# Performance work log

Hardware: AMD Instinct MI355X
Metric: run time of the kernel (lower is better)

## Reference

```python
import jax, jax.numpy as jnp
import numpy as np

B, T, D = 128, 256, 1024

def setup_inputs() -> dict:
    key = jax.random.key(0)
    ks = jax.random.split(key, 7)
    s = 1.0 / np.sqrt(D)
    return {
        "inputs": jax.random.normal(ks[0], (B, T, D), dtype=jnp.float32),
        "Wk": jax.random.uniform(ks[1], (D, D), jnp.float32, -s, s),
        "bk": jax.random.uniform(ks[2], (D,), jnp.float32, -s, s),
        "Wq": jax.random.uniform(ks[3], (D, D), jnp.float32, -s, s),
        "bq": jax.random.uniform(ks[4], (D,), jnp.float32, -s, s),
        "Wv": jax.random.uniform(ks[5], (D, D), jnp.float32, -s, s),
        "bv": jax.random.uniform(ks[6], (D,), jnp.float32, -s, s),
    }

def reference(inputs, Wk, bk, Wq, bq, Wv, bv):
    # torch.nn.Linear: y = x @ W.T + b
    keys = inputs @ Wk.T + bk        # [B, T, D]
    queries = inputs @ Wq.T + bq     # [B, T, D]
    values = inputs @ Wv.T + bv      # [B, T, D]
    scale = 1.0 / jnp.sqrt(jnp.float32(inputs.shape[-1]))
    scores = jnp.einsum('btd,bsd->bts', queries, keys) * scale  # [B, T, T]
    t = inputs.shape[1]
    causal = jnp.tril(jnp.ones((t, t), dtype=bool))
    scores = jnp.where(causal, scores, -jnp.inf)
    probs = jax.nn.softmax(scores, axis=-1)
    return jnp.einsum('bts,bsd->btd', probs, values)
```

## Files before the change

kernel.cpp:

```cpp
#include <hip/hip_runtime.h>
#include <hip/hip_bf16.h>


typedef __attribute__((ext_vector_type(4))) float f32x4;
typedef __attribute__((ext_vector_type(8))) short s16x8;
typedef unsigned short u16;

__device__ inline u16 f2bf(float f) {
    union { __hip_bfloat16 h; u16 u; } c;
    c.h = __float2bfloat16(f);
    return c.u;
}

__device__ __forceinline__ void stage16(const void* g, void* l) {
    __builtin_amdgcn_global_load_lds((const __attribute__((address_space(1))) void*)g,
                                     (__attribute__((address_space(3))) void*)l, 16, 0, 0);
}

#define MFMA(a_, b_, c_) (c_) = __builtin_amdgcn_mfma_f32_16x16x32_bf16((a_), (b_), (c_), 0, 0, 0)

__global__ __launch_bounds__(256) void cvt_f32_bf16(const float* __restrict__ in,
                                                    u16* __restrict__ out, int n4) {
    int stride = gridDim.x * blockDim.x;
    for (int i = blockIdx.x * blockDim.x + threadIdx.x; i < n4; i += stride) {
        float4 v = reinterpret_cast<const float4*>(in)[i];
        ushort4 o = make_ushort4(f2bf(v.x), f2bf(v.y), f2bf(v.z), f2bf(v.w));
        reinterpret_cast<ushort4*>(out)[i] = o;
    }
}

__global__ __launch_bounds__(512, 4) void qkv128(const u16* __restrict__ X, const u16* __restrict__ W3,
                                                 const float* __restrict__ biasK,
                                                 const float* __restrict__ biasQ,
                                                 const float* __restrict__ biasV,
                                                 u16* __restrict__ Kb, u16* __restrict__ Qb,
                                                 u16* __restrict__ Vt) {
    __shared__ char lds[49152];

    const int bid = blockIdx.x;
    const int swz = (bid & 7) * 384 + (bid >> 3);
    const int mt = swz / 12, nt2 = swz % 12;
    const int nmat = nt2 >> 2, ncol = nt2 & 3;
    const u16* Asrc = X + (size_t)mt * 128 * 1024;
    const u16* Bsrc = W3 + (size_t)nmat * 1048576 + (size_t)ncol * 256 * 1024;

    const int tid  = threadIdx.x;
    const int lane = tid & 63, w = tid >> 6;
    const int wr = w >> 2, wc = w & 3;
    const int l15 = lane & 15, l16 = lane >> 4;

    const int rdoff = l15 * 64 + (((l16 ^ ((l15 >> 1) & 3)) & 3) << 4);
    const int aoff = wr * 4096 + rdoff;
    const int boff = 8192 + wc * 4096 + rdoff;

    const int srow = tid >> 2, sslot = tid & 3;
    const int scol = (sslot ^ ((srow >> 1) & 3)) * 8;
    const u16* asrcp  = Asrc + (size_t)srow * 1024 + scol;
    const u16* bsrcp0 = Bsrc + (size_t)srow * 1024 + scol;
    const u16* bsrcp1 = Bsrc + (size_t)(srow + 128) * 1024 + scol;

    f32x4 acc[4][4] = {};

#define STG(u_) do {                                                              \
        char* bb_ = lds + (((u_) & 1) * 24576) + w * 1024;                        \
        const size_t ko_ = (size_t)(u_) * 32;                                     \
        stage16(asrcp  + ko_, bb_);                                               \
        stage16(bsrcp0 + ko_, bb_ + 8192);                                        \
        stage16(bsrcp1 + ko_, bb_ + 16384);                                       \
    } while (0)

    STG(0);
    asm volatile("s_waitcnt vmcnt(0)" ::: "memory");
    __builtin_amdgcn_s_barrier();

    for (int u = 0; u < 32; ++u) {
        if (u < 31) STG(u + 1);
        const char* bp = lds + (u & 1) * 24576;
        s16x8 a[4], b[4];
#pragma unroll
        for (int fm = 0; fm < 4; ++fm) a[fm] = *(const s16x8*)(bp + aoff + fm * 1024);
#pragma unroll
        for (int fn = 0; fn < 4; ++fn) b[fn] = *(const s16x8*)(bp + boff + fn * 1024);
        __builtin_amdgcn_s_setprio(1);
#pragma unroll
        for (int fm = 0; fm < 4; ++fm)
#pragma unroll
            for (int fn = 0; fn < 4; ++fn)
                MFMA(a[fm], b[fn], acc[fm][fn]);
        __builtin_amdgcn_s_setprio(0);
        asm volatile("s_waitcnt vmcnt(0)" ::: "memory");
        __builtin_amdgcn_s_barrier();
    }
#undef STG

    const float* bias = (nmat == 0) ? biasK : (nmat == 1) ? biasQ : biasV;
    u16* outKQ = (nmat == 0) ? Kb : Qb;
    const int r0 = l16 << 2;
#pragma unroll
    for (int m = 0; m < 4; ++m) {
#pragma unroll
        for (int n = 0; n < 4; ++n) {
            const int col = ncol * 256 + wc * 64 + n * 16 + l15;
            const float bvv = bias[col];
            const int rbase = mt * 128 + wr * 64 + m * 16 + r0;
#pragma unroll
            for (int j = 0; j < 4; ++j) {
                const int row = rbase + j;
                const u16 hb = f2bf(acc[m][n][j] + bvv);
                if (nmat == 2) {
                    const int b2 = row >> 8, tt2 = row & 255;
                    Vt[(size_t)b2 * 262144 + (size_t)col * 256 + tt2] = hb;
                } else {
                    outKQ[(size_t)row * 1024 + col] = hb;
                }
            }
        }
    }
}

__device__ inline void gemm_mainloop(const u16* __restrict__ Ap, const u16* __restrict__ Bp,
                                     int lda, int ldb, int kLen,
                                     u16* As, u16* Bs, f32x4 (&acc)[4][4]) {
    const int tid  = threadIdx.x;
    const int lane = tid & 63;
    const int wr   = (tid >> 7) & 1;
    const int wc   = (tid >> 6) & 1;
    const int sr   = tid >> 3;
    const int sc   = (tid & 7) << 3;

    for (int k0 = 0; k0 < kLen; k0 += 64) {
#pragma unroll
        for (int it = 0; it < 4; ++it) {
            int r = it * 32 + sr;
            *reinterpret_cast<s16x8*>(&As[r * 64 + sc]) =
                *reinterpret_cast<const s16x8*>(&Ap[(size_t)r * lda + k0 + sc]);
            *reinterpret_cast<s16x8*>(&Bs[r * 64 + sc]) =
                *reinterpret_cast<const s16x8*>(&Bp[(size_t)r * ldb + k0 + sc]);
        }
        __syncthreads();
#pragma unroll
        for (int kk = 0; kk < 64; kk += 32) {
            const int kcol = kk + (lane >> 4) * 8;
            s16x8 a[4], bfr[4];
#pragma unroll
            for (int m = 0; m < 4; ++m)
                a[m] = *reinterpret_cast<const s16x8*>(&As[(wr * 64 + m * 16 + (lane & 15)) * 64 + kcol]);
#pragma unroll
            for (int n = 0; n < 4; ++n)
                bfr[n] = *reinterpret_cast<const s16x8*>(&Bs[(wc * 64 + n * 16 + (lane & 15)) * 64 + kcol]);
#pragma unroll
            for (int m = 0; m < 4; ++m)
#pragma unroll
                for (int n = 0; n < 4; ++n)
                    acc[m][n] = __builtin_amdgcn_mfma_f32_16x16x32_bf16(a[m], bfr[n], acc[m][n], 0, 0, 0);
        }
        __syncthreads();
    }
}

__global__ __launch_bounds__(256) void scores_gemm(const u16* __restrict__ Qb,
                                                   const u16* __restrict__ Kb,
                                                   float* __restrict__ S) {
    __shared__ u16 As[128 * 64];
    __shared__ u16 Bs[128 * 64];
    const int bid = blockIdx.x;
    const int b   = bid / 3;
    const int rem = bid % 3;
    const int ti  = (rem == 0) ? 0 : 1;
    const int si  = (rem == 2) ? 1 : 0;
    const u16* Ap = Qb + ((size_t)b * 256 + (size_t)ti * 128) * 1024;
    const u16* Bp = Kb + ((size_t)b * 256 + (size_t)si * 128) * 1024;

    f32x4 acc[4][4] = {};
    gemm_mainloop(Ap, Bp, 1024, 1024, 1024, As, Bs, acc);

    const int tid  = threadIdx.x;
    const int lane = tid & 63;
    const int wr   = (tid >> 7) & 1;
    const int wc   = (tid >> 6) & 1;
    const int r0 = (lane >> 4) << 2;
    const int c0 = lane & 15;
    const float scale = 0.03125f;
#pragma unroll
    for (int m = 0; m < 4; ++m) {
#pragma unroll
        for (int n = 0; n < 4; ++n) {
            const int s = si * 128 + wc * 64 + n * 16 + c0;
#pragma unroll
            for (int j = 0; j < 4; ++j) {
                const int t = ti * 128 + wr * 64 + m * 16 + r0 + j;
                float v = acc[m][n][j] * scale;
                if (s > t) v = -__builtin_inff();
                S[(size_t)b * 65536 + (size_t)t * 256 + s] = v;
            }
        }
    }
}

__global__ __launch_bounds__(256) void softmax_p(const float* __restrict__ S, u16* __restrict__ P) {
    const int row  = blockIdx.x * 4 + (threadIdx.x >> 6);
    const int lane = threadIdx.x & 63;
    const int b = row >> 8, t = row & 255;
    const float* Sp = S + (size_t)b * 65536 + (size_t)t * 256;
    const int s0 = lane * 4;
    float4 v = reinterpret_cast<const float4*>(Sp)[lane];
    const float NEG = -__builtin_inff();
    float x0 = (s0 + 0 <= t) ? v.x : NEG;
    float x1 = (s0 + 1 <= t) ? v.y : NEG;
    float x2 = (s0 + 2 <= t) ? v.z : NEG;
    float x3 = (s0 + 3 <= t) ? v.w : NEG;
    float mx = fmaxf(fmaxf(x0, x1), fmaxf(x2, x3));
#pragma unroll
    for (int off = 1; off < 64; off <<= 1) mx = fmaxf(mx, __shfl_xor(mx, off, 64));
    float e0 = (s0 + 0 <= t) ? __expf(x0 - mx) : 0.f;
    float e1 = (s0 + 1 <= t) ? __expf(x1 - mx) : 0.f;
    float e2 = (s0 + 2 <= t) ? __expf(x2 - mx) : 0.f;
    float e3 = (s0 + 3 <= t) ? __expf(x3 - mx) : 0.f;
    float sum = e0 + e1 + e2 + e3;
#pragma unroll
    for (int off = 1; off < 64; off <<= 1) sum += __shfl_xor(sum, off, 64);
    const float inv = 1.0f / sum;
    ushort4 o = make_ushort4(f2bf(e0 * inv), f2bf(e1 * inv), f2bf(e2 * inv), f2bf(e3 * inv));
    reinterpret_cast<ushort4*>(P + (size_t)row * 256)[lane] = o;
}

__global__ __launch_bounds__(256) void pv_gemm(const u16* __restrict__ P, const u16* __restrict__ Vt,
                                               float* __restrict__ O) {
    __shared__ u16 As[128 * 64];
    __shared__ u16 Bs[128 * 64];
    const int bid = blockIdx.x;
    const int b   = bid >> 4;
    const int r   = bid & 15;
    const int mt  = r >> 3;
    const int ntl = r & 7;
    const u16* Ap = P + (size_t)b * 65536 + (size_t)mt * 128 * 256;
    const u16* Bp = Vt + (size_t)b * 262144 + (size_t)ntl * 128 * 256;
    const int kmax = (mt + 1) * 128;

    f32x4 acc[4][4] = {};
    gemm_mainloop(Ap, Bp, 256, 256, kmax, As, Bs, acc);

    const int tid  = threadIdx.x;
    const int lane = tid & 63;
    const int wr   = (tid >> 7) & 1;
    const int wc   = (tid >> 6) & 1;
    const int r0 = (lane >> 4) << 2;
    const int c0 = lane & 15;
#pragma unroll
    for (int m = 0; m < 4; ++m) {
#pragma unroll
        for (int n = 0; n < 4; ++n) {
            const int d = ntl * 128 + wc * 64 + n * 16 + c0;
#pragma unroll
            for (int j = 0; j < 4; ++j) {
                const int t = mt * 128 + wr * 64 + m * 16 + r0 + j;
                O[((size_t)b * 256 + t) * 1024 + d] = acc[m][n][j];
            }
        }
    }
}

extern "C" void kernel_launch(void* const* d_in, const int* in_sizes, int n_in,
                              void* d_out, int out_size, void* d_ws, size_t ws_size,
                              hipStream_t stream) {
    (void)in_sizes; (void)n_in; (void)out_size; (void)ws_size;
    const float* x  = (const float*)d_in[0];
    const float* Wk = (const float*)d_in[1];
    const float* bk = (const float*)d_in[2];
    const float* Wq = (const float*)d_in[3];
    const float* bq = (const float*)d_in[4];
    const float* Wv = (const float*)d_in[5];
    const float* bv = (const float*)d_in[6];
    float* out = (float*)d_out;
    char* ws = (char*)d_ws;

    u16*   xb = (u16*)(ws + 0);
    u16*   Wb = (u16*)(ws + 67108864);
    u16*   Kb = (u16*)(ws + 73400320);
    u16*   Qb = (u16*)(ws + 140509184);
    u16*   Vt = (u16*)(ws + 207618048);
    float* S  = (float*)(ws + 0);
    u16*   P  = (u16*)(ws + 33554432);

    cvt_f32_bf16<<<2048, 256, 0, stream>>>(x, xb, 33554432 / 4);
    cvt_f32_bf16<<<512, 256, 0, stream>>>(Wk, Wb, 1048576 / 4);
    cvt_f32_bf16<<<512, 256, 0, stream>>>(Wq, Wb + 1048576, 1048576 / 4);
    cvt_f32_bf16<<<512, 256, 0, stream>>>(Wv, Wb + 2097152, 1048576 / 4);
    qkv128<<<3072, 512, 0, stream>>>(xb, Wb, bk, bq, bv, Kb, Qb, Vt);
    scores_gemm<<<384, 256, 0, stream>>>(Qb, Kb, S);
    softmax_p<<<8192, 256, 0, stream>>>(S, P);
    pv_gemm<<<2048, 256, 0, stream>>>(P, Vt, out);
}
```

Before: 425.1 us.

## Fuse causal scores GEMM with softmax and triple-buffer QKV projection loads

Replaces the separate scores GEMM and softmax kernels with one kernel. Each block computes a full 128-row strip of causal scores, then does the row max and sum reduction through shared memory and writes bf16 probabilities directly. This removes the fp32 score matrix write and re-read and one kernel launch. The cost is fewer blocks, uneven work between the two row tiles, and more accumulator registers. Separately, the QKV GEMM moves from a double-buffered to a triple-buffered LDS pipeline with a deeper vmcnt wait, which grows LDS per block and may lower occupancy.

```diff
diff --git a/kernel.cpp b/kernel.cpp
--- a/kernel.cpp
+++ b/kernel.cpp
@@ -35,7 +35,7 @@
                                                  const float* __restrict__ biasV,
                                                  u16* __restrict__ Kb, u16* __restrict__ Qb,
                                                  u16* __restrict__ Vt) {
-    __shared__ char lds[49152];
+    __shared__ char lds[73728];
 
     const int bid = blockIdx.x;
     const int swz = (bid & 7) * 384 + (bid >> 3);
@@ -62,20 +62,20 @@
     f32x4 acc[4][4] = {};
 
 #define STG(u_) do {                                                              \
-        char* bb_ = lds + (((u_) & 1) * 24576) + w * 1024;                        \
+        char* bb_ = lds + (((u_) % 3) * 24576) + w * 1024;                        \
         const size_t ko_ = (size_t)(u_) * 32;                                     \
         stage16(asrcp  + ko_, bb_);                                               \
         stage16(bsrcp0 + ko_, bb_ + 8192);                                        \
         stage16(bsrcp1 + ko_, bb_ + 16384);                                       \
     } while (0)
 
-    STG(0);
-    asm volatile("s_waitcnt vmcnt(0)" ::: "memory");
+    STG(0); STG(1);
+    asm volatile("s_waitcnt vmcnt(3)" ::: "memory");
     __builtin_amdgcn_s_barrier();
 
     for (int u = 0; u < 32; ++u) {
-        if (u < 31) STG(u + 1);
-        const char* bp = lds + (u & 1) * 24576;
+        if (u < 30) STG(u + 2);
+        const char* bp = lds + (u % 3) * 24576;
         s16x8 a[4], b[4];
 #pragma unroll
         for (int fm = 0; fm < 4; ++fm) a[fm] = *(const s16x8*)(bp + aoff + fm * 1024);
@@ -88,7 +88,8 @@
             for (int fn = 0; fn < 4; ++fn)
                 MFMA(a[fm], b[fn], acc[fm][fn]);
         __builtin_amdgcn_s_setprio(0);
-        asm volatile("s_waitcnt vmcnt(0)" ::: "memory");
+        if (u < 30) asm volatile("s_waitcnt vmcnt(3)" ::: "memory");
+        else        asm volatile("s_waitcnt vmcnt(0)" ::: "memory");
         __builtin_amdgcn_s_barrier();
     }
 #undef STG
@@ -118,6 +119,143 @@
     }
 }
 
+__global__ __launch_bounds__(256) void scores_sm(const u16* __restrict__ Qb,
+                                                 const u16* __restrict__ Kb,
+                                                 u16* __restrict__ P) {
+    __shared__ u16 As[128 * 64];
+    __shared__ u16 Bs[256 * 64];
+    __shared__ float redM[2][128];
+    __shared__ float redS[2][128];
+
+    const int bid = blockIdx.x;
+    const int b = bid >> 1, ti = bid & 1;
+    const int nB = 1 + ti;
+    const u16* Ap = Qb + ((size_t)b * 256 + (size_t)ti * 128) * 1024;
+    const u16* Bp = Kb + (size_t)b * 256 * 1024;
+
+    const int tid  = threadIdx.x;
+    const int lane = tid & 63;
+    const int wr   = (tid >> 7) & 1;
+    const int wc   = (tid >> 6) & 1;
+    const int sr   = tid >> 3;
+    const int sc   = (tid & 7) << 3;
+
+    f32x4 acc[2][4][4] = {};
+
+    for (int k0 = 0; k0 < 1024; k0 += 64) {
+#pragma unroll
+        for (int it = 0; it < 4; ++it) {
+            int r = it * 32 + sr;
+            *reinterpret_cast<s16x8*>(&As[r * 64 + sc]) =
+                *reinterpret_cast<const s16x8*>(&Ap[(size_t)r * 1024 + k0 + sc]);
+        }
+#pragma unroll
+        for (int it = 0; it < 8; ++it) {
+            if (it < 4 * nB) {
+                int r = it * 32 + sr;
+                *reinterpret_cast<s16x8*>(&Bs[r * 64 + sc]) =
+                    *reinterpret_cast<const s16x8*>(&Bp[(size_t)r * 1024 + k0 + sc]);
+            }
+        }
+        __syncthreads();
+#pragma unroll
+        for (int kk = 0; kk < 64; kk += 32) {
+            const int kcol = kk + (lane >> 4) * 8;
+            s16x8 a[4], bb[2][4];
+#pragma unroll
+            for (int m = 0; m < 4; ++m)
+                a[m] = *reinterpret_cast<const s16x8*>(&As[(wr * 64 + m * 16 + (lane & 15)) * 64 + kcol]);
+#pragma unroll
+            for (int nt = 0; nt < 2; ++nt)
+                if (nt < nB)
+#pragma unroll
+                    for (int n = 0; n < 4; ++n)
+                        bb[nt][n] = *reinterpret_cast<const s16x8*>(&Bs[(nt * 128 + wc * 64 + n * 16 + (lane & 15)) * 64 + kcol]);
+#pragma unroll
+            for (int nt = 0; nt < 2; ++nt)
+                if (nt < nB)
+#pragma unroll
+                    for (int m = 0; m < 4; ++m)
+#pragma unroll
+                        for (int n = 0; n < 4; ++n)
+                            MFMA(a[m], bb[nt][n], acc[nt][m][n]);
+        }
+        __syncthreads();
+    }
+
+    const int r0 = (lane >> 4) << 2;
+    const int c0 = lane & 15;
+    const float scale = 0.03125f;
+    const float NEG = -__builtin_inff();
+
+#pragma unroll
+    for (int m = 0; m < 4; ++m) {
+#pragma unroll
+        for (int j = 0; j < 4; ++j) {
+            const int rr = wr * 64 + m * 16 + r0 + j;
+            const int t_ = ti * 128 + rr;
+            float mx = NEG;
+#pragma unroll
+            for (int nt = 0; nt < 2; ++nt)
+                if (nt < nB)
+#pragma unroll
+                    for (int n = 0; n < 4; ++n) {
+                        const int s_ = nt * 128 + wc * 64 + n * 16 + c0;
+                        float v = acc[nt][m][n][j] * scale;
+                        v = (s_ <= t_) ? v : NEG;
+                        acc[nt][m][n][j] = v;
+                        mx = fmaxf(mx, v);
+                    }
+#pragma unroll
+            for (int off = 1; off < 16; off <<= 1) mx = fmaxf(mx, __shfl_xor(mx, off, 64));
+            if (c0 == 0) redM[wc][rr] = mx;
+        }
+    }
+    __syncthreads();
+
+#pragma unroll
+    for (int m = 0; m < 4; ++m) {
+#pragma unroll
+        for (int j = 0; j < 4; ++j) {
+            const int rr = wr * 64 + m * 16 + r0 + j;
+            const float MX = fmaxf(redM[0][rr], redM[1][rr]);
+            float s = 0.f;
+#pragma unroll
+            for (int nt = 0; nt < 2; ++nt)
+                if (nt < nB)
+#pragma unroll
+                    for (int n = 0; n < 4; ++n) {
+                        float e = __expf(acc[nt][m][n][j] - MX);
+                        acc[nt][m][n][j] = e;
+                        s += e;
+                    }
+#pragma unroll
+            for (int off = 1; off < 16; off <<= 1) s += __shfl_xor(s, off, 64);
+            if (c0 == 0) redS[wc][rr] = s;
+        }
+    }
+    __syncthreads();
+
+#pragma unroll
+    for (int m = 0; m < 4; ++m) {
+#pragma unroll
+        for (int j = 0; j < 4; ++j) {
+            const int rr = wr * 64 + m * 16 + r0 + j;
+            const int t_ = ti * 128 + rr;
+            const float inv = 1.0f / (redS[0][rr] + redS[1][rr]);
+            u16* Pr = P + (size_t)b * 65536 + (size_t)t_ * 256;
+#pragma unroll
+            for (int nt = 0; nt < 2; ++nt)
+                if (nt < nB)
+#pragma unroll
+                    for (int n = 0; n < 4; ++n) {
+                        const int s_ = nt * 128 + wc * 64 + n * 16 + c0;
+                        Pr[s_] = f2bf(acc[nt][m][n][j] * inv);
+                    }
+        }
+    }
+}
+
 __device__ inline void gemm_mainloop(const u16* __restrict__ Ap, const u16* __restrict__ Bp,
                                      int lda, int ldb, int kLen,
                                      u16* As, u16* Bs, f32x4 (&acc)[4][4]) {
@@ -156,72 +294,6 @@
         }
         __syncthreads();
     }
-}
-
-__global__ __launch_bounds__(256) void scores_gemm(const u16* __restrict__ Qb,
-                                                   const u16* __restrict__ Kb,
-                                                   float* __restrict__ S) {
-    __shared__ u16 As[128 * 64];
-    __shared__ u16 Bs[128 * 64];
-    const int bid = blockIdx.x;
-    const int b   = bid / 3;
-    const int rem = bid % 3;
-    const int ti  = (rem == 0) ? 0 : 1;
-    const int si  = (rem == 2) ? 1 : 0;
-    const u16* Ap = Qb + ((size_t)b * 256 + (size_t)ti * 128) * 1024;
-    const u16* Bp = Kb + ((size_t)b * 256 + (size_t)si * 128) * 1024;
-
-    f32x4 acc[4][4] = {};
-    gemm_mainloop(Ap, Bp, 1024, 1024, 1024, As, Bs, acc);
-
-    const int tid  = threadIdx.x;
-    const int lane = tid & 63;
-    const int wr   = (tid >> 7) & 1;
-    const int wc   = (tid >> 6) & 1;
-    const int r0 = (lane >> 4) << 2;
-    const int c0 = lane & 15;
-    const float scale = 0.03125f;
-#pragma unroll
-    for (int m = 0; m < 4; ++m) {
-#pragma unroll
-        for (int n = 0; n < 4; ++n) {
-            const int s = si * 128 + wc * 64 + n * 16 + c0;
-#pragma unroll
-            for (int j = 0; j < 4; ++j) {
-                const int t = ti * 128 + wr * 64 + m * 16 + r0 + j;
-                float v = acc[m][n][j] * scale;
-                if (s > t) v = -__builtin_inff();
-                S[(size_t)b * 65536 + (size_t)t * 256 + s] = v;
-            }
-        }
-    }
-}
-
-__global__ __launch_bounds__(256) void softmax_p(const float* __restrict__ S, u16* __restrict__ P) {
-    const int row  = blockIdx.x * 4 + (threadIdx.x >> 6);
-    const int lane = threadIdx.x & 63;
-    const int b = row >> 8, t = row & 255;
-    const float* Sp = S + (size_t)b * 65536 + (size_t)t * 256;
-    const int s0 = lane * 4;
-    float4 v = reinterpret_cast<const float4*>(Sp)[lane];
-    const float NEG = -__builtin_inff();
-    float x0 = (s0 + 0 <= t) ? v.x : NEG;
-    float x1 = (s0 + 1 <= t) ? v.y : NEG;
-    float x2 = (s0 + 2 <= t) ? v.z : NEG;
-    float x3 = (s0 + 3 <= t) ? v.w : NEG;
-    float mx = fmaxf(fmaxf(x0, x1), fmaxf(x2, x3));
-#pragma unroll
-    for (int off = 1; off < 64; off <<= 1) mx = fmaxf(mx, __shfl_xor(mx, off, 64));
-    float e0 = (s0 + 0 <= t) ? __expf(x0 - mx) : 0.f;
-    float e1 = (s0 + 1 <= t) ? __expf(x1 - mx) : 0.f;
-    float e2 = (s0 + 2 <= t) ? __expf(x2 - mx) : 0.f;
-    float e3 = (s0 + 3 <= t) ? __expf(x3 - mx) : 0.f;
-    float sum = e0 + e1 + e2 + e3;
-#pragma unroll
-    for (int off = 1; off < 64; off <<= 1) sum += __shfl_xor(sum, off, 64);
-    const float inv = 1.0f / sum;
-    ushort4 o = make_ushort4(f2bf(e0 * inv), f2bf(e1 * inv), f2bf(e2 * inv), f2bf(e3 * inv));
-    reinterpret_cast<ushort4*>(P + (size_t)row * 256)[lane] = o;
 }
 
 __global__ __launch_bounds__(256) void pv_gemm(const u16* __restrict__ P, const u16* __restrict__ Vt,
@@ -279,7 +351,6 @@
     u16*   Kb = (u16*)(ws + 73400320);
     u16*   Qb = (u16*)(ws + 140509184);
     u16*   Vt = (u16*)(ws + 207618048);
-    float* S  = (float*)(ws + 0);
     u16*   P  = (u16*)(ws + 33554432);
 
     cvt_f32_bf16<<<2048, 256, 0, stream>>>(x, xb, 33554432 / 4);
@@ -287,7 +358,6 @@
     cvt_f32_bf16<<<512, 256, 0, stream>>>(Wq, Wb + 1048576, 1048576 / 4);
     cvt_f32_bf16<<<512, 256, 0, stream>>>(Wv, Wb + 2097152, 1048576 / 4);
     qkv128<<<3072, 512, 0, stream>>>(xb, Wb, bk, bq, bv, Kb, Qb, Vt);
-    scores_gemm<<<384, 256, 0, stream>>>(Qb, Kb, S);
-    softmax_p<<<8192, 256, 0, stream>>>(S, P);
+    scores_sm<<<256, 256, 0, stream>>>(Qb, Kb, P);
     pv_gemm<<<2048, 256, 0, stream>>>(P, Vt, out);
 }
```

Measured after the change: 473.8 us. 1.11x slower.
